# Performance work log

Measured on AMD Instinct MI355X. Metric: run time of the kernel, lower is better.

Reference implementation:

```python
import jax, jax.numpy as jnp
import numpy as np

N_NODES = 100000
N_EDGES = 3200000
IN_DIM = 128
HID = 64
OUT_DIM = 128
N_GRAPHS = 8


def _gcn_conv(x, W, b, src, dst, w, n):
    # GCNConv (PyG default): add self-loops (weight 1), symmetric normalization
    loop = jnp.arange(n)
    src2 = jnp.concatenate([src, loop])
    dst2 = jnp.concatenate([dst, loop])
    w2 = jnp.concatenate([w, jnp.ones((n,), x.dtype)])
    deg = jax.ops.segment_sum(w2, dst2, num_segments=n)
    dinv = jnp.where(deg > 0, jax.lax.rsqrt(deg), 0.0)
    norm = dinv[src2] * w2 * dinv[dst2]            # [E+N]
    h = x @ W                                      # transform before gather
    msg = h[src2] * norm[:, None]                  # gather + scale
    out = jax.ops.segment_sum(msg, dst2, num_segments=n)  # scatter-add
    return out + b


def setup_inputs() -> dict:
    key = jax.random.key(0)
    ks = jax.random.split(key, 10)
    x = jax.random.normal(ks[0], (N_NODES, IN_DIM), dtype=jnp.float32)
    edge_index = jax.random.randint(ks[1], (2, N_EDGES), 0, N_NODES, dtype=jnp.int64)
    edge_weight = jax.random.uniform(ks[2], (N_EDGES,), dtype=jnp.float32)
    batch = jnp.sort(jax.random.randint(ks[3], (N_NODES,), 0, N_GRAPHS, dtype=jnp.int64))
    # params (glorot-ish scale)
    W1 = jax.random.normal(ks[4], (IN_DIM, HID), dtype=jnp.float32) / np.sqrt(IN_DIM)
    b1 = jnp.zeros((HID,), jnp.float32)
    W2 = jax.random.normal(ks[5], (HID, HID), dtype=jnp.float32) / np.sqrt(HID)
    b2 = jnp.zeros((HID,), jnp.float32)
    Wfc = jax.random.normal(ks[6], (HID, OUT_DIM), dtype=jnp.float32) / np.sqrt(HID)
    bfc = jnp.zeros((OUT_DIM,), jnp.float32)
    return {"x": x, "edge_index": edge_index, "edge_weight": edge_weight,
            "batch": batch, "W1": W1, "b1": b1, "W2": W2, "b2": b2,
            "Wfc": Wfc, "bfc": bfc}


def reference(x, edge_index, edge_weight, batch, W1, b1, W2, b2, Wfc, bfc):
    src, dst = edge_index[0], edge_index[1]
    n = x.shape[0]
    h = _gcn_conv(x, W1, b1, src, dst, edge_weight, n)
    h = jax.nn.relu(h)
    h = _gcn_conv(h, W2, b2, src, dst, edge_weight, n)
    # global_mean_pool over batch ids
    sums = jax.ops.segment_sum(h, batch, num_segments=N_GRAPHS)
    cnts = jax.ops.segment_sum(jnp.ones((n,), h.dtype), batch, num_segments=N_GRAPHS)
    pooled = sums / jnp.maximum(cnts, 1.0)[:, None]
    return pooled @ Wfc + bfc
```

## Files before the change

kernel.cpp:

```cpp
#include <hip/hip_runtime.h>

#define IN_DIM 128
#define HID 64
#define OUT_DIM 128
#define NGRAPH 8

#define CHUNK 8192
#define BSH 9
#define BSZ 512

typedef unsigned long long u64;
typedef unsigned int u32;
typedef __attribute__((ext_vector_type(8))) short short8;
typedef __attribute__((ext_vector_type(4))) float f32x4;

__device__ inline short bf16b(float f) {
    u32 u = __float_as_uint(f);
    return (short)((u + 0x7FFFu + ((u >> 16) & 1u)) >> 16);
}
__device__ inline u32 pack_bf16(float a, float b) {
    u32 ua = (__float_as_uint(a) + 0x8000u) >> 16;
    u32 ub = (__float_as_uint(b) + 0x8000u) & 0xFFFF0000u;
    return ua | ub;
}
__device__ inline float bf16_lo(u32 v) { return __uint_as_float(v << 16); }
__device__ inline float bf16_hi(u32 v) { return __uint_as_float(v & 0xFFFF0000u); }

__global__ __launch_bounds__(256) void bhist_kernel(const int* __restrict__ dst,
                                                    u32* __restrict__ hist,
                                                    int E, int nchunk, int nbuck) {
    __shared__ u32 h[256];
    for (int i = threadIdx.x; i < 256; i += 256) h[i] = 0;
    __syncthreads();
    int c = blockIdx.x;
    int beg = c * CHUNK, end = min(beg + CHUNK, E);
    for (int i = beg + threadIdx.x; i < end; i += 256)
        atomicAdd(&h[dst[i] >> BSH], 1u);
    __syncthreads();
    for (int b = threadIdx.x; b < nbuck; b += 256)
        hist[(size_t)b * nchunk + c] = h[b];
}

__global__ __launch_bounds__(512) void scanS1(u32* __restrict__ hist, u32* __restrict__ tot,
                                              int nchunk, int nbuck) {
    __shared__ u32 sm[512];
    int b = blockIdx.x;
    u32 v = (threadIdx.x < nchunk) ? hist[(size_t)b * nchunk + threadIdx.x] : 0;
    sm[threadIdx.x] = v;
    __syncthreads();
    for (int off = 1; off < 512; off <<= 1) {
        u32 t = (threadIdx.x >= off) ? sm[threadIdx.x - off] : 0;
        __syncthreads();
        sm[threadIdx.x] += t;
        __syncthreads();
    }
    if (threadIdx.x < nchunk) hist[(size_t)b * nchunk + threadIdx.x] = sm[threadIdx.x] - v;
    if (threadIdx.x == 511) tot[b] = sm[511];
}

__global__ __launch_bounds__(512) void scanS2(const u32* __restrict__ tot, u32* __restrict__ base,
                                              int nbuck) {
    __shared__ u32 sm[512];
    u32 v = (threadIdx.x < nbuck) ? tot[threadIdx.x] : 0;
    sm[threadIdx.x] = v;
    __syncthreads();
    for (int off = 1; off < 512; off <<= 1) {
        u32 t = (threadIdx.x >= off) ? sm[threadIdx.x - off] : 0;
        __syncthreads();
        sm[threadIdx.x] += t;
        __syncthreads();
    }
    if ((int)threadIdx.x <= nbuck) base[threadIdx.x] = sm[threadIdx.x] - v;
}

__global__ __launch_bounds__(256) void bin_kernel(const int* __restrict__ src,
                                                  const int* __restrict__ dst,
                                                  const float* __restrict__ ew,
                                                  const u32* __restrict__ offs,
                                                  const u32* __restrict__ base,
                                                  int2* __restrict__ bse,
                                                  int E, int nchunk, int nbuck) {
    __shared__ u32 cur[256];
    int c = blockIdx.x;
    for (int b = threadIdx.x; b < nbuck; b += 256)
        cur[b] = base[b] + offs[(size_t)b * nchunk + c];
    __syncthreads();
    int beg = c * CHUNK, end = min(beg + CHUNK, E);
    for (int i = beg + threadIdx.x; i < end; i += 256) {
        int d = dst[i];
        int b = d >> BSH;
        u32 slot = atomicAdd(&cur[b], 1u);
        bse[slot] = make_int2(src[i] | ((d & (BSZ - 1)) << 17), __float_as_int(ew[i]));
    }
}

__global__ __launch_bounds__(256) void csr_kernel(const int2* __restrict__ bse,
                                                  const u32* __restrict__ base,
                                                  int* __restrict__ row_ptr,
                                                  float* __restrict__ dinv,
                                                  int2* __restrict__ edges, int N) {
    __shared__ u32 cnt[BSZ];
    __shared__ float wdeg[BSZ];
    __shared__ u32 rp[BSZ];
    int b = blockIdx.x;
    int beg = base[b], end = base[b + 1];
    int i0 = threadIdx.x, i1 = threadIdx.x + 256;
    cnt[i0] = 0; cnt[i1] = 0; wdeg[i0] = 0.f; wdeg[i1] = 0.f;
    __syncthreads();
    for (int i = beg + threadIdx.x; i < end; i += 256) {
        int2 e = bse[i];
        int dl = (e.x >> 17) & (BSZ - 1);
        atomicAdd(&cnt[dl], 1u);
        atomicAdd(&wdeg[dl], __int_as_float(e.y));
    }
    __syncthreads();
    u32 v0 = cnt[i0], v1 = cnt[i1];
    rp[i0] = v0; rp[i1] = v1;
    __syncthreads();
    for (int off = 1; off < BSZ; off <<= 1) {
        u32 t0 = (i0 >= off) ? rp[i0 - off] : 0;
        u32 t1 = (i1 >= off) ? rp[i1 - off] : 0;
        __syncthreads();
        rp[i0] += t0; rp[i1] += t1;
        __syncthreads();
    }
    int node0 = b * BSZ + i0, node1 = b * BSZ + i1;
    if (node0 <= N) row_ptr[node0] = beg + (int)(rp[i0] - v0);
    if (node1 <= N) row_ptr[node1] = beg + (int)(rp[i1] - v1);
    if (node0 < N) dinv[node0] = rsqrtf(wdeg[i0] + 1.0f);
    if (node1 < N) dinv[node1] = rsqrtf(wdeg[i1] + 1.0f);
    __syncthreads();
    cnt[i0] = rp[i0] - v0;
    cnt[i1] = rp[i1] - v1;
    __syncthreads();
    for (int i = beg + threadIdx.x; i < end; i += 256) {
        int2 e = bse[i];
        int dl = (e.x >> 17) & (BSZ - 1);
        u32 r = atomicAdd(&cnt[dl], 1u);
        edges[beg + r] = make_int2(e.x & 0x1FFFF, e.y);
    }
}

__global__ __launch_bounds__(256) void gemm1_kernel(const float* __restrict__ x,
                                                    const float* __restrict__ W1,
                                                    const float* __restrict__ dinv,
                                                    u32* __restrict__ hb, int N) {
    int wave = threadIdx.x >> 6, lane = threadIdx.x & 63;
    int col = lane & 15, kg = lane >> 4;
    int rowbase = blockIdx.x * 64 + wave * 16;

    short8 bW[4][4];
#pragma unroll
    for (int ks = 0; ks < 4; ++ks)
#pragma unroll
        for (int nt = 0; nt < 4; ++nt) {
            const float* wp = W1 + (size_t)(ks * 32 + kg * 8) * HID + nt * 16 + col;
            short8 f;
#pragma unroll
            for (int j = 0; j < 8; ++j) f[j] = bf16b(wp[j * HID]);
            bW[ks][nt] = f;
        }

    f32x4 acc[4];
#pragma unroll
    for (int nt = 0; nt < 4; ++nt) acc[nt] = (f32x4){0.f, 0.f, 0.f, 0.f};

    int arow = rowbase + col;
    if (arow >= N) arow = N - 1;
    const float4* xr = reinterpret_cast<const float4*>(x + (size_t)arow * IN_DIM);
#pragma unroll
    for (int ks = 0; ks < 4; ++ks) {
        float4 xa = xr[ks * 8 + kg * 2];
        float4 xb = xr[ks * 8 + kg * 2 + 1];
        short8 a;
        a[0] = bf16b(xa.x); a[1] = bf16b(xa.y); a[2] = bf16b(xa.z); a[3] = bf16b(xa.w);
        a[4] = bf16b(xb.x); a[5] = bf16b(xb.y); a[6] = bf16b(xb.z); a[7] = bf16b(xb.w);
#pragma unroll
        for (int nt = 0; nt < 4; ++nt)
            acc[nt] = __builtin_amdgcn_mfma_f32_16x16x32_bf16(a, bW[ks][nt], acc[nt], 0, 0, 0);
    }

#pragma unroll
    for (int r = 0; r < 4; ++r) {
        int row = rowbase + kg * 4 + r;
        if (row < N) {
            float di = dinv[row];
            hb[(size_t)row * 32 + col]      = pack_bf16(acc[0][r] * di, acc[2][r] * di);
            hb[(size_t)row * 32 + col + 16] = pack_bf16(acc[1][r] * di, acc[3][r] * di);
        }
    }
}

__global__ void agg_kernel(const int* __restrict__ row_ptr, const int2* __restrict__ edges,
                           const float* __restrict__ dinv, const u32* __restrict__ hb,
                           u32* __restrict__ aggb, int N) {
    int gid = blockIdx.x * blockDim.x + threadIdx.x;
    int node = gid >> 6, lane = gid & 63;
    if (node >= N) return;
    int half = lane >> 5, l = lane & 31;
    int beg = row_ptr[node], end = row_ptr[node + 1];
    int mid = beg + ((end - beg + 1) >> 1);
    int lo = half ? mid : beg;
    int hi = half ? end : mid;
    float ax = 0.f, ay = 0.f;
    if (half == 0) {
        u32 hv = hb[(size_t)node * 32 + l];
        ax = bf16_lo(hv);
        ay = bf16_hi(hv);
    }
    int i = lo;
    for (; i + 8 <= hi; i += 8) {
        int2 e0 = edges[i+0], e1 = edges[i+1], e2 = edges[i+2], e3 = edges[i+3];
        int2 e4 = edges[i+4], e5 = edges[i+5], e6 = edges[i+6], e7 = edges[i+7];
        u32 h0 = hb[(size_t)e0.x * 32 + l], h1 = hb[(size_t)e1.x * 32 + l];
        u32 h2 = hb[(size_t)e2.x * 32 + l], h3 = hb[(size_t)e3.x * 32 + l];
        u32 h4 = hb[(size_t)e4.x * 32 + l], h5 = hb[(size_t)e5.x * 32 + l];
        u32 h6 = hb[(size_t)e6.x * 32 + l], h7 = hb[(size_t)e7.x * 32 + l];
        float c0 = __int_as_float(e0.y), c1 = __int_as_float(e1.y);
        float c2 = __int_as_float(e2.y), c3 = __int_as_float(e3.y);
        float c4 = __int_as_float(e4.y), c5 = __int_as_float(e5.y);
        float c6 = __int_as_float(e6.y), c7 = __int_as_float(e7.y);
        ax += c0 * bf16_lo(h0); ay += c0 * bf16_hi(h0);
        ax += c1 * bf16_lo(h1); ay += c1 * bf16_hi(h1);
        ax += c2 * bf16_lo(h2); ay += c2 * bf16_hi(h2);
        ax += c3 * bf16_lo(h3); ay += c3 * bf16_hi(h3);
        ax += c4 * bf16_lo(h4); ay += c4 * bf16_hi(h4);
        ax += c5 * bf16_lo(h5); ay += c5 * bf16_hi(h5);
        ax += c6 * bf16_lo(h6); ay += c6 * bf16_hi(h6);
        ax += c7 * bf16_lo(h7); ay += c7 * bf16_hi(h7);
    }
    if (i < hi) {
        int2 e[8];
#pragma unroll
        for (int k = 0; k < 8; ++k) {
            int j = i + k;
            e[k] = edges[j < hi ? j : i];
            if (j >= hi) e[k].y = 0;
        }
        u32 hh[8];
#pragma unroll
        for (int k = 0; k < 8; ++k) hh[k] = hb[(size_t)e[k].x * 32 + l];
#pragma unroll
        for (int k = 0; k < 8; ++k) {
            float c = __int_as_float(e[k].y);
            ax += c * bf16_lo(hh[k]);
            ay += c * bf16_hi(hh[k]);
        }
    }
    ax += __shfl_xor(ax, 32);
    ay += __shfl_xor(ay, 32);
    float di = dinv[node];
    if (lane < 32) aggb[(size_t)node * 32 + l] = pack_bf16(di * ax, di * ay);
}

__global__ __launch_bounds__(256) void gemm2_kernel(const u32* __restrict__ aggb,
                                                    const float* __restrict__ b1,
                                                    const float* __restrict__ W2,
                                                    const float* __restrict__ dinv,
                                                    u32* __restrict__ hb, int N) {
    int wave = threadIdx.x >> 6, lane = threadIdx.x & 63;
    int col = lane & 15, kg = lane >> 4;
    int rowbase = blockIdx.x * 64 + wave * 16;

    short8 bW[2][4];
#pragma unroll
    for (int ks = 0; ks < 2; ++ks)
#pragma unroll
        for (int nt = 0; nt < 4; ++nt) {
            const float* wp = W2 + (size_t)(ks * 32 + kg * 8) * HID + nt * 16 + col;
            short8 f;
#pragma unroll
            for (int j = 0; j < 8; ++j) f[j] = bf16b(wp[j * HID]);
            bW[ks][nt] = f;
        }

    f32x4 acc[4];
#pragma unroll
    for (int nt = 0; nt < 4; ++nt) acc[nt] = (f32x4){0.f, 0.f, 0.f, 0.f};

    int arow = rowbase + col;
    if (arow >= N) arow = N - 1;
    const u32* ar = aggb + (size_t)arow * 32 + kg * 8;
    u32 w[8];
#pragma unroll
    for (int j = 0; j < 8; ++j) w[j] = ar[j];
#pragma unroll
    for (int ks = 0; ks < 2; ++ks) {
        short8 a;
#pragma unroll
        for (int j = 0; j < 8; ++j) {
            float f = ks ? bf16_hi(w[j]) : bf16_lo(w[j]);
            a[j] = bf16b(fmaxf(f + b1[ks * 32 + kg * 8 + j], 0.f));
        }
#pragma unroll
        for (int nt = 0; nt < 4; ++nt)
            acc[nt] = __builtin_amdgcn_mfma_f32_16x16x32_bf16(a, bW[ks][nt], acc[nt], 0, 0, 0);
    }

#pragma unroll
    for (int r = 0; r < 4; ++r) {
        int row = rowbase + kg * 4 + r;
        if (row < N) {
            float di = dinv[row];
            hb[(size_t)row * 32 + col]      = pack_bf16(acc[0][r] * di, acc[2][r] * di);
            hb[(size_t)row * 32 + col + 16] = pack_bf16(acc[1][r] * di, acc[3][r] * di);
        }
    }
}

__global__ void pool_kernel(const u32* __restrict__ aggb, const int* __restrict__ batch,
                            float* __restrict__ pooled, float* __restrict__ cnt,
                            int N, int chunk) {
    int wid = (blockIdx.x * blockDim.x + threadIdx.x) >> 6;
    int lane = threadIdx.x & 63;
    int w = lane & 31, hi = lane >> 5;
    int feat = w + hi * 32;
    int start = wid * chunk;
    if (start >= N) return;
    int end = min(start + chunk, N);
    float acc = 0.f, fc = 0.f;
    int cur = batch[start];
    for (int n = start; n < end; ++n) {
        int g = batch[n];
        if (g != cur) {
            atomicAdd(&pooled[cur * HID + feat], acc);
            if (lane == 0) atomicAdd(&cnt[cur], fc);
            cur = g; acc = 0.f; fc = 0.f;
        }
        u32 hv = aggb[(size_t)n * 32 + w];
        acc += hi ? bf16_hi(hv) : bf16_lo(hv);
        fc += 1.f;
    }
    atomicAdd(&pooled[cur * HID + feat], acc);
    if (lane == 0) atomicAdd(&cnt[cur], fc);
}

__global__ void final_kernel(const float* __restrict__ pooled, const float* __restrict__ cnt,
                             const float* __restrict__ b2, const float* __restrict__ Wfc,
                             const float* __restrict__ bfc, float* __restrict__ out) {
    int idx = blockIdx.x * blockDim.x + threadIdx.x;
    if (idx >= NGRAPH * OUT_DIM) return;
    int g = idx >> 7, o = idx & 127;
    float inv = 1.0f / fmaxf(cnt[g], 1.0f);
    float acc = 0.f;
#pragma unroll
    for (int k = 0; k < HID; ++k)
        acc += (pooled[g * HID + k] * inv + b2[k]) * Wfc[k * OUT_DIM + o];
    out[idx] = acc + bfc[o];
}

extern "C" void kernel_launch(void* const* d_in, const int* in_sizes, int n_in,
                              void* d_out, int out_size, void* d_ws, size_t ws_size,
                              hipStream_t stream) {
    const float* x    = (const float*)d_in[0];
    const int*   ei   = (const int*)d_in[1];
    const float* ew   = (const float*)d_in[2];
    const int*   bat  = (const int*)d_in[3];
    const float* W1   = (const float*)d_in[4];
    const float* b1   = (const float*)d_in[5];
    const float* W2   = (const float*)d_in[6];
    const float* b2   = (const float*)d_in[7];
    const float* Wfc  = (const float*)d_in[8];
    const float* bfc  = (const float*)d_in[9];
    float* out = (float*)d_out;

    const int N = in_sizes[0] / IN_DIM;
    const int E = in_sizes[2];
    const int* src = ei;
    const int* dst = ei + E;

    const int nbuck  = (N + BSZ - 1) >> BSH;
    const int nchunk = (E + CHUNK - 1) / CHUNK;

    char* ws = (char*)d_ws;
    size_t off = 0;
    auto alloc = [&](size_t bytes) {
        char* p = ws + off;
        off += (bytes + 255) / 256 * 256;
        return p;
    };
    u32*   hist    = (u32*)  alloc((size_t)nbuck * nchunk * 4);
    u32*   tot     = (u32*)  alloc(512 * 4);
    u32*   base    = (u32*)  alloc(512 * 4);
    int*   row_ptr = (int*)  alloc((size_t)(N + 1) * 4);
    float* dinv    = (float*)alloc((size_t)N * 4);
    float* pooled  = (float*)alloc((NGRAPH * HID + NGRAPH) * 4);
    float* cnt     = pooled + NGRAPH * HID;
    int2*  bse     = (int2*) alloc((size_t)E * 8);
    int2*  edges   = (int2*) alloc((size_t)E * 8);
    u32*   hb      = (u32*)  alloc((size_t)N * 32 * 4);
    u32*   aggb    = (u32*)  alloc((size_t)N * 32 * 4);

    hipMemsetAsync(pooled, 0, (NGRAPH * HID + NGRAPH) * 4, stream);

    bhist_kernel<<<nchunk, 256, 0, stream>>>(dst, hist, E, nchunk, nbuck);
    scanS1<<<nbuck, 512, 0, stream>>>(hist, tot, nchunk, nbuck);
    scanS2<<<1, 512, 0, stream>>>(tot, base, nbuck);
    bin_kernel<<<nchunk, 256, 0, stream>>>(src, dst, ew, hist, base, bse, E, nchunk, nbuck);
    csr_kernel<<<nbuck, 256, 0, stream>>>(bse, base, row_ptr, dinv, edges, N);

    int gemmBlocks = (N + 63) / 64;
    int rowBlocks = (int)(((size_t)N * 64 + 255) / 256);

    gemm1_kernel<<<gemmBlocks, 256, 0, stream>>>(x, W1, dinv, hb, N);
    agg_kernel<<<rowBlocks, 256, 0, stream>>>(row_ptr, edges, dinv, hb, aggb, N);

    gemm2_kernel<<<gemmBlocks, 256, 0, stream>>>(aggb, b1, W2, dinv, hb, N);
    agg_kernel<<<rowBlocks, 256, 0, stream>>>(row_ptr, edges, dinv, hb, aggb, N);

    const int POOL_WAVES = 1024;
    int chunk = (N + POOL_WAVES - 1) / POOL_WAVES;
    pool_kernel<<<POOL_WAVES / 4, 256, 0, stream>>>(aggb, bat, pooled, cnt, N, chunk);

    final_kernel<<<(NGRAPH * OUT_DIM + 255) / 256, 256, 0, stream>>>(pooled, cnt, b2, Wfc, bfc, out);
}
```

Before: 312.3 us.

## Stage binned edges in shared memory to coalesce bucket scatter writes

```diff
diff --git a/kernel.cpp b/kernel.cpp
--- a/kernel.cpp
+++ b/kernel.cpp
@@ -5,7 +5,7 @@
 #define OUT_DIM 128
 #define NGRAPH 8
 
-#define CHUNK 8192
+#define CHUNK 4096
 #define BSH 9
 #define BSZ 512
 
@@ -30,7 +30,7 @@
                                                     u32* __restrict__ hist,
                                                     int E, int nchunk, int nbuck) {
     __shared__ u32 h[256];
-    for (int i = threadIdx.x; i < 256; i += 256) h[i] = 0;
+    h[threadIdx.x] = 0;
     __syncthreads();
     int c = blockIdx.x;
     int beg = c * CHUNK, end = min(beg + CHUNK, E);
@@ -43,19 +43,23 @@
 
 __global__ __launch_bounds__(512) void scanS1(u32* __restrict__ hist, u32* __restrict__ tot,
                                               int nchunk, int nbuck) {
-    __shared__ u32 sm[512];
+    __shared__ u32 sm[1024];
     int b = blockIdx.x;
-    u32 v = (threadIdx.x < nchunk) ? hist[(size_t)b * nchunk + threadIdx.x] : 0;
-    sm[threadIdx.x] = v;
-    __syncthreads();
-    for (int off = 1; off < 512; off <<= 1) {
-        u32 t = (threadIdx.x >= off) ? sm[threadIdx.x - off] : 0;
-        __syncthreads();
-        sm[threadIdx.x] += t;
-        __syncthreads();
-    }
-    if (threadIdx.x < nchunk) hist[(size_t)b * nchunk + threadIdx.x] = sm[threadIdx.x] - v;
-    if (threadIdx.x == 511) tot[b] = sm[511];
+    int i0 = threadIdx.x, i1 = threadIdx.x + 512;
+    u32 v0 = (i0 < nchunk) ? hist[(size_t)b * nchunk + i0] : 0;
+    u32 v1 = (i1 < nchunk) ? hist[(size_t)b * nchunk + i1] : 0;
+    sm[i0] = v0; sm[i1] = v1;
+    __syncthreads();
+    for (int off = 1; off < 1024; off <<= 1) {
+        u32 t0 = (i0 >= off) ? sm[i0 - off] : 0;
+        u32 t1 = (i1 >= off) ? sm[i1 - off] : 0;
+        __syncthreads();
+        sm[i0] += t0; sm[i1] += t1;
+        __syncthreads();
+    }
+    if (i0 < nchunk) hist[(size_t)b * nchunk + i0] = sm[i0] - v0;
+    if (i1 < nchunk) hist[(size_t)b * nchunk + i1] = sm[i1] - v1;
+    if (threadIdx.x == 511) tot[b] = sm[1023];
 }
 
 __global__ __launch_bounds__(512) void scanS2(const u32* __restrict__ tot, u32* __restrict__ base,
@@ -80,17 +84,47 @@
                                                   const u32* __restrict__ base,
                                                   int2* __restrict__ bse,
                                                   int E, int nchunk, int nbuck) {
-    __shared__ u32 cur[256];
+    __shared__ u32 lcnt[256];
+    __shared__ u32 lpos[256];
+    __shared__ u32 gbase[256];
+    __shared__ int2 buf[CHUNK];
+    __shared__ unsigned char bb[CHUNK];
+
     int c = blockIdx.x;
-    for (int b = threadIdx.x; b < nbuck; b += 256)
-        cur[b] = base[b] + offs[(size_t)b * nchunk + c];
-    __syncthreads();
     int beg = c * CHUNK, end = min(beg + CHUNK, E);
+    lcnt[threadIdx.x] = 0;
+    __syncthreads();
+    for (int i = beg + threadIdx.x; i < end; i += 256)
+        atomicAdd(&lcnt[dst[i] >> BSH], 1u);
+    __syncthreads();
+    u32 v = lcnt[threadIdx.x];
+    lpos[threadIdx.x] = v;
+    __syncthreads();
+    for (int off = 1; off < 256; off <<= 1) {
+        u32 t = (threadIdx.x >= off) ? lpos[threadIdx.x - off] : 0;
+        __syncthreads();
+        lpos[threadIdx.x] += t;
+        __syncthreads();
+    }
+    u32 excl = lpos[threadIdx.x] - v;
+    __syncthreads();
+    lpos[threadIdx.x] = excl;
+    lcnt[threadIdx.x] = excl;
+    if (threadIdx.x < (u32)nbuck)
+        gbase[threadIdx.x] = base[threadIdx.x] + offs[(size_t)threadIdx.x * nchunk + c];
+    __syncthreads();
     for (int i = beg + threadIdx.x; i < end; i += 256) {
         int d = dst[i];
         int b = d >> BSH;
-        u32 slot = atomicAdd(&cur[b], 1u);
-        bse[slot] = make_int2(src[i] | ((d & (BSZ - 1)) << 17), __float_as_int(ew[i]));
+        u32 p = atomicAdd(&lcnt[b], 1u);
+        buf[p] = make_int2(src[i] | ((d & (BSZ - 1)) << 17), __float_as_int(ew[i]));
+        bb[p] = (unsigned char)b;
+    }
+    __syncthreads();
+    int tot = end - beg;
+    for (int j = threadIdx.x; j < tot; j += 256) {
+        int b = bb[j];
+        bse[gbase[b] + j - lpos[b]] = buf[j];
     }
 }
 
```

Result: faster. 301.6 us (-3.4%).
